# Performance work log

Measured on AMD Instinct MI355X. Metric: run time of the kernel, lower is better.

The kernel has to match this reference:

```python
import jax, jax.numpy as jnp
import numpy as np

# dims (match init_kwargs / input_specs)
D = 768      # embed_dim
H = 12       # num query heads
G = 4        # num kv groups
E = 8        # num experts
K = 2        # experts per token
F = 4 * D    # ffn hidden dim
B, S, T = 2, 1024, 1024
DH = D // H  # head dim = 64
EPS = 1e-6


def setup_inputs() -> dict:
    key = jax.random.key(0)
    ks = jax.random.split(key, 16)

    def p(k, shape, scale=0.02):
        return jax.random.normal(k, shape, jnp.float32) * scale

    inp = {}
    inp['x'] = jax.random.normal(ks[0], (B, S, D), jnp.float32)
    inp['encoder_context'] = jax.random.normal(ks[1], (B, T, D), jnp.float32)
    for n in ('ln1', 'ln2', 'ln3'):
        inp[n + '_scale'] = jnp.ones((D,), jnp.float32)
        inp[n + '_bias'] = jnp.zeros((D,), jnp.float32)
    i = 2
    for pre in ('sa', 'ca'):
        inp[pre + '_wq'] = p(ks[i], (D, H * DH)); i += 1
        inp[pre + '_bq'] = jnp.zeros((H * DH,), jnp.float32)
        inp[pre + '_wk'] = p(ks[i], (D, G * DH)); i += 1
        inp[pre + '_bk'] = jnp.zeros((G * DH,), jnp.float32)
        inp[pre + '_wv'] = p(ks[i], (D, G * DH)); i += 1
        inp[pre + '_bv'] = jnp.zeros((G * DH,), jnp.float32)
        inp[pre + '_wo'] = p(ks[i], (H * DH, D)); i += 1
        inp[pre + '_bo'] = jnp.zeros((D,), jnp.float32)
    inp['gate_w'] = p(ks[i], (D, E)); i += 1
    inp['gate_b'] = jnp.zeros((E,), jnp.float32)
    inp['w1'] = p(ks[i], (E, D, F)); i += 1
    inp['b1'] = jnp.zeros((E, F), jnp.float32)
    inp['w2'] = p(ks[i], (E, F, D)); i += 1
    inp['b2'] = jnp.zeros((E, D), jnp.float32)
    return inp


def _ln(x, scale, bias):
    mu = jnp.mean(x, axis=-1, keepdims=True)
    var = jnp.mean(jnp.square(x - mu), axis=-1, keepdims=True)
    return (x - mu) * jax.lax.rsqrt(var + EPS) * scale + bias


def _gqa(q_in, kv_in, wq, bq, wk, bk, wv, bv, wo, bo, causal):
    Bq, Sq, _ = q_in.shape
    Skv = kv_in.shape[1]
    q = (q_in @ wq + bq).reshape(Bq, Sq, H, DH)
    k = (kv_in @ wk + bk).reshape(Bq, Skv, G, DH)
    v = (kv_in @ wv + bv).reshape(Bq, Skv, G, DH)
    rep = H // G
    k = jnp.repeat(k, rep, axis=2)  # [B,Skv,H,DH]
    v = jnp.repeat(v, rep, axis=2)
    scores = jnp.einsum('bqhd,bkhd->bhqk', q, k) / jnp.sqrt(jnp.asarray(DH, q.dtype))
    if causal:
        cmask = jnp.tril(jnp.ones((Sq, Skv), bool))
        scores = jnp.where(cmask[None, None], scores, jnp.finfo(scores.dtype).min)
    attn = jax.nn.softmax(scores, axis=-1)
    out = jnp.einsum('bhqk,bkhd->bqhd', attn, v).reshape(Bq, Sq, H * DH)
    return out @ wo + bo


def _moe(x, gate_w, gate_b, w1, b1, w2, b2):
    logits = x @ gate_w + gate_b                      # [B,S,E]
    probs = jax.nn.softmax(logits, axis=-1)
    top_v, top_i = jax.lax.top_k(probs, K)            # [B,S,K]
    top_v = top_v / jnp.sum(top_v, axis=-1, keepdims=True)
    combine = jnp.sum(jax.nn.one_hot(top_i, E, dtype=x.dtype) * top_v[..., None], axis=-2)  # [B,S,E]
    h = jax.nn.gelu(jnp.einsum('bsd,edf->ebsf', x, w1) + b1[:, None, None, :])
    y = jnp.einsum('ebsf,efd->ebsd', h, w2) + b2[:, None, None, :]
    return jnp.einsum('ebsd,bse->bsd', y, combine)


def reference(x, encoder_context,
              ln1_scale, ln1_bias, ln2_scale, ln2_bias, ln3_scale, ln3_bias,
              sa_wq, sa_bq, sa_wk, sa_bk, sa_wv, sa_bv, sa_wo, sa_bo,
              ca_wq, ca_bq, ca_wk, ca_bk, ca_wv, ca_bv, ca_wo, ca_bo,
              gate_w, gate_b, w1, b1, w2, b2):
    xn = _ln(x, ln1_scale, ln1_bias)
    x = x + _gqa(xn, xn, sa_wq, sa_bq, sa_wk, sa_bk, sa_wv, sa_bv, sa_wo, sa_bo, causal=True)
    xn = _ln(x, ln2_scale, ln2_bias)
    x = x + _gqa(xn, encoder_context, ca_wq, ca_bq, ca_wk, ca_bk, ca_wv, ca_bv, ca_wo, ca_bo, causal=False)
    xn = _ln(x, ln3_scale, ln3_bias)
    x = x + _moe(xn, gate_w, gate_b, w1, b1, w2, b2)
    return x
```

## Files before the change

### kernel.cpp

```cpp
#include <hip/hip_runtime.h>

#define DEV __device__ __forceinline__

typedef __attribute__((ext_vector_type(4))) float f32x4;
typedef __attribute__((ext_vector_type(8))) short short8;
typedef __attribute__((ext_vector_type(4))) unsigned int u32x4;
typedef __attribute__((ext_vector_type(4))) unsigned short us16x4;

#define D_ 768
#define S_ 1024
#define B_ 2
#define H_ 12
#define G_ 4
#define DH_ 64
#define E_ 8
#define F_ 3072
#define NTOK (B_*S_)

#define GLDS16(g, l) __builtin_amdgcn_global_load_lds( \
    (const __attribute__((address_space(1))) void*)(g), \
    (__attribute__((address_space(3))) void*)(l), 16, 0, 0)

DEV unsigned short f2bf(float f){
  unsigned int b = __float_as_uint(f);
  b += 0x7FFFu + ((b >> 16) & 1u);
  return (unsigned short)(b >> 16);
}
DEV float bf2f(unsigned short h){ return __uint_as_float(((unsigned int)h) << 16); }
DEV unsigned int splitbf_pack(float v){
  unsigned short h = f2bf(v);
  unsigned short l = f2bf(v - bf2f(h));
  return (unsigned int)h | ((unsigned int)l << 16);
}

DEV short8 lds_swz(const unsigned short* base, int row, int chunk){
  return *(const short8*)((const char*)base + row*128 + (((chunk ^ (row & 7)) << 4)));
}
DEV short8 lds_swz32(const unsigned short* base, int row, int chunk){
  return *(const short8*)((const char*)base + row*64 + (((chunk ^ (row & 3)) << 4)));
}

DEV void swz_decode(int Fb, int nPanels, int& m, int& panel){
  int xcd = Fb & 7;
  int a = Fb >> 3;
  int mi = a & 3;
  int pid = (a >> 2)*8 + xcd;
  m = (pid / nPanels)*4 + mi;
  panel = pid % nPanels;
}

__global__ __launch_bounds__(256) void tcast_kernel(const float* __restrict__ W,
                                                    unsigned short* __restrict__ Wh,
                                                    unsigned short* __restrict__ Wl,
                                                    int K, int N){
  __shared__ float tile[32][33];
  long long zoff = (long long)blockIdx.z * K * N;
  const float* Wz = W + zoff;
  int n0 = blockIdx.x*32, k0 = blockIdx.y*32;
  int tx = threadIdx.x, ty = threadIdx.y;
  #pragma unroll
  for (int i=0;i<4;i++){
    int r = ty + i*8;
    tile[r][tx] = Wz[(long long)(k0+r)*N + n0 + tx];
  }
  __syncthreads();
  #pragma unroll
  for (int i=0;i<4;i++){
    int r = ty + i*8;
    float v = tile[tx][r];
    unsigned int hl = splitbf_pack(v);
    long long o = zoff + (long long)(n0+r)*K + k0 + tx;
    Wh[o] = (unsigned short)(hl & 0xFFFFu);
    if (Wl) Wl[o] = (unsigned short)(hl >> 16);
  }
}

struct TC4 {
  const float* s[4];
  unsigned short* h[4];
  unsigned short* l[4];
};
__global__ __launch_bounds__(256) void tcast4_kernel(TC4 tc, int K, int N){
  __shared__ float tile[32][33];
  int zi = blockIdx.z;
  const float* Wz = tc.s[zi];
  unsigned short* Wh = tc.h[zi];
  unsigned short* Wl = tc.l[zi];
  int n0 = blockIdx.x*32, k0 = blockIdx.y*32;
  int tx = threadIdx.x, ty = threadIdx.y;
  #pragma unroll
  for (int i=0;i<4;i++){
    int r = ty + i*8;
    tile[r][tx] = Wz[(long long)(k0+r)*N + n0 + tx];
  }
  __syncthreads();
  #pragma unroll
  for (int i=0;i<4;i++){
    int r = ty + i*8;
    float v = tile[tx][r];
    unsigned int hl = splitbf_pack(v);
    long long o = (long long)(n0+r)*K + k0 + tx;
    Wh[o] = (unsigned short)(hl & 0xFFFFu);
    Wl[o] = (unsigned short)(hl >> 16);
  }
}

__global__ void split_rows(const float* __restrict__ in, int ld, int width,
                           unsigned short* __restrict__ hi, unsigned short* __restrict__ lo){
  long long t = blockIdx.x;
  int c = threadIdx.x*4;
  f32x4 v = *(const f32x4*)(in + t*ld + c);
  unsigned int p0 = splitbf_pack(v.x), p1 = splitbf_pack(v.y);
  unsigned int p2 = splitbf_pack(v.z), p3 = splitbf_pack(v.w);
  us16x4 h, l;
  h.x=(unsigned short)p0; l.x=(unsigned short)(p0>>16);
  h.y=(unsigned short)p1; l.y=(unsigned short)(p1>>16);
  h.z=(unsigned short)p2; l.z=(unsigned short)(p2>>16);
  h.w=(unsigned short)p3; l.w=(unsigned short)(p3>>16);
  *(us16x4*)(hi + t*width + c) = h;
  *(us16x4*)(lo + t*width + c) = l;
}

__global__ void concat_bias(const float* __restrict__ b0, int n0,
                            const float* __restrict__ b1, int n1,
                            const float* __restrict__ b2, int n2,
                            float* __restrict__ out){
  int i = blockIdx.x*256 + threadIdx.x;
  if (i < n0) out[i] = b0[i];
  else if (i < n0+n1) out[i] = b1[i-n0];
  else if (i < n0+n1+n2) out[i] = b2[i-n0-n1];
}

__global__ __launch_bounds__(256) void ln_kernel(const float* __restrict__ x,
                                                 const float* __restrict__ sc,
                                                 const float* __restrict__ bi,
                                                 unsigned short* __restrict__ outh,
                                                 unsigned short* __restrict__ outl,
                                                 float* __restrict__ outf){
  __shared__ float red[8];
  long long row = blockIdx.x;
  const float* xr = x + row*D_;
  int tid = threadIdx.x;
  float v0 = xr[tid], v1 = xr[tid+256], v2 = xr[tid+512];
  float s = v0+v1+v2;
  float q = v0*v0 + v1*v1 + v2*v2;
  #pragma unroll
  for (int off=32; off; off>>=1){ s += __shfl_xor(s, off); q += __shfl_xor(q, off); }
  int lane = tid & 63, w = tid >> 6;
  if (lane == 0){ red[w] = s; red[4+w] = q; }
  __syncthreads();
  s = red[0]+red[1]+red[2]+red[3];
  q = red[4]+red[5]+red[6]+red[7];
  float mu  = s * (1.0f/D_);
  float var = q * (1.0f/D_) - mu*mu;
  float rstd = rsqrtf(var + 1e-6f);
  #pragma unroll
  for (int i=0;i<3;i++){
    int idx = tid + 256*i;
    float vv = (i==0) ? v0 : (i==1) ? v1 : v2;
    float o = (vv - mu)*rstd*sc[idx] + bi[idx];
    unsigned int pk = splitbf_pack(o);
    outh[row*D_ + idx] = (unsigned short)(pk & 0xFFFFu);
    if (outl) outl[row*D_ + idx] = (unsigned short)(pk >> 16);
    if (outf) outf[row*D_ + idx] = o;
  }
}

__global__ __launch_bounds__(256) void gemm3(
    int nX,
    const unsigned short* __restrict__ Ah, const unsigned short* __restrict__ Al, int lda,
    const unsigned short* __restrict__ Wh, const unsigned short* __restrict__ Wl, int K,
    const float* __restrict__ bias,
    const float* __restrict__ resid, int ldr,
    float* __restrict__ Cf, int ldc)
{
  __shared__ __align__(16) unsigned short AshH[128*64];
  __shared__ __align__(16) unsigned short AshL[128*64];
  __shared__ __align__(16) unsigned short BshH[64*64];
  __shared__ __align__(16) unsigned short BshL[64*64];
  int mB, panel;
  swz_decode(blockIdx.x, nX, mB, panel);
  const int r0 = mB*128;
  const int n0 = panel*64;
  const int tid = threadIdx.x;
  const int lane = tid & 63;
  const int wv = tid >> 6;
  const int wr = (wv>>1)*64, wc = (wv&1)*32;
  const int l15 = lane & 15, l4 = lane >> 4;
  const int sr = lane >> 3;
  const int sc = (lane & 7) ^ sr;

  f32x4 acc[4][2];
  #pragma unroll
  for (int i=0;i<4;i++)
    #pragma unroll
    for (int j=0;j<2;j++) acc[i][j] = (f32x4){0.f,0.f,0.f,0.f};

  for (int k0 = 0; k0 < K; k0 += 64){
    #pragma unroll
    for (int i=0;i<4;i++){
      int seg = wv*4 + i;
      long long src = (long long)(r0 + seg*8 + sr)*lda + k0 + sc*8;
      GLDS16(Ah + src, AshH + seg*8*64);
      GLDS16(Al + src, AshL + seg*8*64);
    }
    #pragma unroll
    for (int i=0;i<2;i++){
      int seg = wv*2 + i;
      long long src = (long long)(n0 + seg*8 + sr)*K + k0 + sc*8;
      GLDS16(Wh + src, BshH + seg*8*64);
      GLDS16(Wl + src, BshL + seg*8*64);
    }
    __syncthreads();
    #pragma unroll
    for (int ks=0; ks<2; ks++){
      int chunk = ks*4 + l4;
      short8 bh[2], bl[2];
      #pragma unroll
      for (int fj=0; fj<2; fj++){
        bh[fj] = lds_swz(BshH, wc + fj*16 + l15, chunk);
        bl[fj] = lds_swz(BshL, wc + fj*16 + l15, chunk);
      }
      #pragma unroll
      for (int fi=0; fi<4; fi++){
        short8 ah = lds_swz(AshH, wr + fi*16 + l15, chunk);
        short8 al = lds_swz(AshL, wr + fi*16 + l15, chunk);
        #pragma unroll
        for (int fj=0; fj<2; fj++){
          acc[fi][fj] = __builtin_amdgcn_mfma_f32_16x16x32_bf16(ah, bh[fj], acc[fi][fj], 0,0,0);
          acc[fi][fj] = __builtin_amdgcn_mfma_f32_16x16x32_bf16(al, bh[fj], acc[fi][fj], 0,0,0);
          acc[fi][fj] = __builtin_amdgcn_mfma_f32_16x16x32_bf16(ah, bl[fj], acc[fi][fj], 0,0,0);
        }
      }
    }
    __syncthreads();
  }

  #pragma unroll
  for (int fi=0; fi<4; fi++)
  #pragma unroll
  for (int fj=0; fj<2; fj++)
  #pragma unroll
  for (int reg=0; reg<4; reg++){
    int r = r0 + wr + fi*16 + l4*4 + reg;
    int col = n0 + wc + fj*16 + l15;
    float val = acc[fi][fj][reg] + bias[col];
    if (resid) val += resid[(long long)r*ldr + col];
    Cf[(long long)r*ldc + col] = val;
  }
}

__global__ __launch_bounds__(256) void gemm_nt128(
    int nX, int nzPerE,
    const unsigned short* __restrict__ A, int lda,
    const unsigned short* __restrict__ Wt, long long wstride,
    const float* __restrict__ bias, int bias_stride,
    const int* __restrict__ counts,
    const int* __restrict__ a_idx, int a_idx_stride,
    const int* __restrict__ row_base,
    float* __restrict__ Cf, long long partStride,
    unsigned short* __restrict__ Cb, int ldc,
    int K, int do_gelu)
{
  __shared__ __align__(16) unsigned short As[2][128*32];
  __shared__ __align__(16) unsigned short Bs[2][128*32];
  int mB, panel;
  swz_decode(blockIdx.x, nX*E_*nzPerE, mB, panel);
  const int n0 = (panel % nX)*128;
  const int zI = panel / nX;
  const int z = zI / nzPerE;
  const int kp = zI % nzPerE;
  const int Mz = counts[z];
  const int r0 = mB*128;
  if (r0 >= Mz) return;
  const int obase = row_base[z];
  const unsigned short* Wz = Wt + (long long)z*wstride;
  const float* bz = bias + (long long)z*bias_stride;
  const int kLen = K / nzPerE;
  const int kBeg = kp * kLen;
  const int tid = threadIdx.x;
  const int lane = tid & 63;
  const int wv = tid >> 6;
  const int wr = (wv>>1)*64, wc = (wv&1)*64;
  const int l15 = lane & 15, l4 = lane >> 4;
  const int r16 = lane >> 2;
  const int sc4 = (lane & 3) ^ (r16 & 3);

  long long arow[2];
  #pragma unroll
  for (int i=0;i<2;i++){
    int seg = wv*2 + i;
    int r = r0 + seg*16 + r16;
    int rcl = (r < Mz) ? r : (Mz-1);
    arow[i] = a_idx ? (long long)a_idx[(long long)z*a_idx_stride + rcl]
                    : (long long)(obase + rcl);
  }

  f32x4 acc[4][4];
  #pragma unroll
  for (int i=0;i<4;i++)
    #pragma unroll
    for (int j=0;j<4;j++) acc[i][j] = (f32x4){0.f,0.f,0.f,0.f};

  auto stage = [&](int buf, int k0){
    #pragma unroll
    for (int i=0;i<2;i++){
      int seg = wv*2 + i;
      GLDS16(A + arow[i]*lda + k0 + sc4*8, &As[buf][seg*512]);
      GLDS16(Wz + (long long)(n0 + seg*16 + r16)*K + k0 + sc4*8, &Bs[buf][seg*512]);
    }
  };

  const int nsteps = kLen >> 5;
  stage(0, kBeg);
  int cur = 0;
  for (int t=0; t<nsteps; t++){
    if (t+1 < nsteps){
      stage(cur^1, kBeg + (t+1)*32);
      asm volatile("s_waitcnt vmcnt(4)" ::: "memory");
    } else {
      asm volatile("s_waitcnt vmcnt(0)" ::: "memory");
    }
    __builtin_amdgcn_s_barrier();
    __builtin_amdgcn_sched_barrier(0);
    {
      short8 a[4], b[4];
      #pragma unroll
      for (int f=0; f<4; f++){
        a[f] = lds_swz32(&As[cur][0], wr + f*16 + l15, l4);
        b[f] = lds_swz32(&Bs[cur][0], wc + f*16 + l15, l4);
      }
      #pragma unroll
      for (int fi=0; fi<4; fi++)
        #pragma unroll
        for (int fj=0; fj<4; fj++)
          acc[fi][fj] = __builtin_amdgcn_mfma_f32_16x16x32_bf16(a[fi], b[fj], acc[fi][fj], 0,0,0);
    }
    __builtin_amdgcn_s_barrier();
    cur ^= 1;
  }

  #pragma unroll
  for (int fi=0; fi<4; fi++)
  #pragma unroll
  for (int fj=0; fj<4; fj++)
  #pragma unroll
  for (int reg=0; reg<4; reg++){
    int r = r0 + wr + fi*16 + l4*4 + reg;
    if (r >= Mz) continue;
    int col = n0 + wc + fj*16 + l15;
    float val = acc[fi][fj][reg] + (kp == 0 ? bz[col] : 0.0f);
    if (do_gelu){
      float xx = val;
      float u = 0.7978845608028654f*(xx + 0.044715f*xx*xx*xx);
      float t = 1.0f - 2.0f/(__expf(2.0f*u) + 1.0f);
      val = 0.5f*xx*(1.0f + t);
    }
    long long orow = (long long)obase + r;
    if (Cf) Cf[kp*partStride + orow*ldc + col] = val;
    if (Cb) Cb[orow*ldc + col] = f2bf(val);
  }
}

__global__ __launch_bounds__(256) void vt_split_kernel(const float* __restrict__ vin,
                                                       int ld, int cofs,
                                                       unsigned short* __restrict__ vth,
                                                       unsigned short* __restrict__ vtl){
  __shared__ float tile[32][33];
  int s0 = blockIdx.x*32, d0 = blockIdx.y*32;
  int bg = blockIdx.z; int b = bg >> 2, g = bg & 3;
  int tx = threadIdx.x, ty = threadIdx.y;
  #pragma unroll
  for (int i=0;i<4;i++){
    int r = ty + i*8;
    tile[r][tx] = vin[(long long)(b*1024 + s0 + r)*ld + cofs + g*64 + d0 + tx];
  }
  __syncthreads();
  #pragma unroll
  for (int i=0;i<4;i++){
    int d = d0 + ty + i*8;
    unsigned int pk = splitbf_pack(tile[tx][ty + i*8]);
    long long o = (long long)(bg*64 + d)*1024 + s0 + tx;
    vth[o] = (unsigned short)(pk & 0xFFFFu);
    vtl[o] = (unsigned short)(pk >> 16);
  }
}

#define AT_LDP 76
__global__ __launch_bounds__(256, 2) void attn_mfma(
    const float* __restrict__ q, int qld,
    const unsigned short* __restrict__ kh, const unsigned short* __restrict__ kl,
    const unsigned short* __restrict__ vth, const unsigned short* __restrict__ vtl,
    unsigned short* __restrict__ ctxh, unsigned short* __restrict__ ctxl, int causal)
{
  __shared__ __align__(16) unsigned short KhS[64*64];
  __shared__ __align__(16) unsigned short KlS[64*64];
  __shared__ __align__(16) unsigned short VhS[64*64];
  __shared__ __align__(16) unsigned short VlS[64*64];
  __shared__ __align__(16) unsigned int   Pp[4][16*AT_LDP];

  const int qblk = blockIdx.x;
  const int h = blockIdx.y;
  const int b = blockIdx.z;
  const int g = h / (H_/G_);
  const int tid = threadIdx.x;
  const int lane = tid & 63;
  const int w = tid >> 6;
  const int l15 = lane & 15;
  const int l4 = lane >> 4;
  const int sr = lane >> 3;
  const int sc = (lane & 7) ^ sr;
  const int qb0 = qblk*64;

  short8 qh[2], ql[2];
  #pragma unroll
  for (int ks=0; ks<2; ks++){
    const float* qp = q + ((long long)(b*S_ + qb0 + w*16 + l15))*qld + h*DH_ + ks*32 + l4*8;
    f32x4 q0 = *(const f32x4*)qp;
    f32x4 q1 = *(const f32x4*)(qp + 4);
    float qq[8] = {q0.x,q0.y,q0.z,q0.w,q1.x,q1.y,q1.z,q1.w};
    #pragma unroll
    for (int j=0;j<8;j++){
      unsigned int pk = splitbf_pack(qq[j]*0.125f);
      qh[ks][j] = (short)(pk & 0xFFFFu);
      ql[ks][j] = (short)(pk >> 16);
    }
  }

  f32x4 o[4];
  #pragma unroll
  for (int fd=0; fd<4; fd++) o[fd] = (f32x4){0.f,0.f,0.f,0.f};
  float m[4]    = {-3.0e38f,-3.0e38f,-3.0e38f,-3.0e38f};
  float lsum[4] = {0.f,0.f,0.f,0.f};

  const int ntiles = causal ? (qblk + 1) : (S_/64);
  for (int kt=0; kt<ntiles; kt++){
    __syncthreads();
    #pragma unroll
    for (int i=0;i<2;i++){
      int seg = w*2 + i;
      int row = seg*8 + sr;
      long long ksrc = (long long)(b*S_ + kt*64 + row)*(G_*DH_) + g*DH_ + sc*8;
      long long vsrc = (long long)((b*G_ + g)*64 + row)*S_ + kt*64 + sc*8;
      GLDS16(kh  + ksrc, KhS + seg*8*64);
      GLDS16(kl  + ksrc, KlS + seg*8*64);
      GLDS16(vth + vsrc, VhS + seg*8*64);
      GLDS16(vtl + vsrc, VlS + seg*8*64);
    }
    __syncthreads();

    f32x4 s[4];
    #pragma unroll
    for (int fj=0; fj<4; fj++) s[fj] = (f32x4){0.f,0.f,0.f,0.f};
    #pragma unroll
    for (int ks=0; ks<2; ks++){
      int chunk = ks*4 + l4;
      #pragma unroll
      for (int fj=0; fj<4; fj++){
        short8 bh = lds_swz(KhS, fj*16 + l15, chunk);
        short8 bl = lds_swz(KlS, fj*16 + l15, chunk);
        s[fj] = __builtin_amdgcn_mfma_f32_16x16x32_bf16(qh[ks], bh, s[fj], 0,0,0);
        s[fj] = __builtin_amdgcn_mfma_f32_16x16x32_bf16(ql[ks], bh, s[fj], 0,0,0);
        s[fj] = __builtin_amdgcn_mfma_f32_16x16x32_bf16(qh[ks], bl, s[fj], 0,0,0);
      }
    }

    if (causal && kt == qblk){
      #pragma unroll
      for (int fj=0; fj<4; fj++){
        int key = kt*64 + fj*16 + l15;
        #pragma unroll
        for (int reg=0; reg<4; reg++){
          int qr = qb0 + w*16 + l4*4 + reg;
          if (key > qr) s[fj][reg] = -3.0e38f;
        }
      }
    }

    float c[4], pmax[4];
    #pragma unroll
    for (int reg=0; reg<4; reg++){
      float mx = fmaxf(fmaxf(s[0][reg], s[1][reg]), fmaxf(s[2][reg], s[3][reg]));
      mx = fmaxf(mx, __shfl_xor(mx, 1));
      mx = fmaxf(mx, __shfl_xor(mx, 2));
      mx = fmaxf(mx, __shfl_xor(mx, 4));
      mx = fmaxf(mx, __shfl_xor(mx, 8));
      float mn = fmaxf(m[reg], mx);
      c[reg] = __expf(m[reg] - mn);
      m[reg] = mn;
      pmax[reg] = mn;
    }
    float psum[4] = {0.f,0.f,0.f,0.f};
    #pragma unroll
    for (int fj=0; fj<4; fj++){
      #pragma unroll
      for (int reg=0; reg<4; reg++){
        float pv = __expf(s[fj][reg] - pmax[reg]);
        psum[reg] += pv;
        Pp[w][(l4*4 + reg)*AT_LDP + fj*16 + l15] = splitbf_pack(pv);
      }
    }
    #pragma unroll
    for (int reg=0; reg<4; reg++){
      float ps = psum[reg];
      ps += __shfl_xor(ps, 1); ps += __shfl_xor(ps, 2);
      ps += __shfl_xor(ps, 4); ps += __shfl_xor(ps, 8);
      lsum[reg] = lsum[reg]*c[reg] + ps;
      o[0][reg] *= c[reg]; o[1][reg] *= c[reg];
      o[2][reg] *= c[reg]; o[3][reg] *= c[reg];
    }

    #pragma unroll
    for (int ks=0; ks<2; ks++){
      int chunk = ks*4 + l4;
      u32x4 pa = *(const u32x4*)&Pp[w][l15*AT_LDP + ks*32 + l4*8];
      u32x4 pb = *(const u32x4*)&Pp[w][l15*AT_LDP + ks*32 + l4*8 + 4];
      short8 ph, pl;
      #pragma unroll
      for (int j=0;j<4;j++){
        ph[j]   = (short)(pa[j] & 0xFFFFu); pl[j]   = (short)(pa[j] >> 16);
        ph[4+j] = (short)(pb[j] & 0xFFFFu); pl[4+j] = (short)(pb[j] >> 16);
      }
      #pragma unroll
      for (int fd=0; fd<4; fd++){
        short8 vh = lds_swz(VhS, fd*16 + l15, chunk);
        short8 vl = lds_swz(VlS, fd*16 + l15, chunk);
        o[fd] = __builtin_amdgcn_mfma_f32_16x16x32_bf16(ph, vh, o[fd], 0,0,0);
        o[fd] = __builtin_amdgcn_mfma_f32_16x16x32_bf16(pl, vh, o[fd], 0,0,0);
        o[fd] = __builtin_amdgcn_mfma_f32_16x16x32_bf16(ph, vl, o[fd], 0,0,0);
      }
    }
  }

  #pragma unroll
  for (int reg=0; reg<4; reg++){
    float inv = 1.0f / lsum[reg];
    long long tok = b*S_ + qb0 + w*16 + l4*4 + reg;
    #pragma unroll
    for (int fd=0; fd<4; fd++){
      unsigned int pk = splitbf_pack(o[fd][reg]*inv);
      long long oidx = tok*D_ + h*DH_ + fd*16 + l15;
      ctxh[oidx] = (unsigned short)(pk & 0xFFFFu);
      ctxl[oidx] = (unsigned short)(pk >> 16);
    }
  }
}

__global__ __launch_bounds__(256) void gate_kernel(const float* __restrict__ xnf,
                                                   const float* __restrict__ gw,
                                                   const float* __restrict__ gb,
                                                   int* __restrict__ counts,
                                                   int* __restrict__ toklist,
                                                   int* __restrict__ route_e,
                                                   int* __restrict__ route_pos,
                                                   float* __restrict__ route_w){
  int t = blockIdx.x*4 + (threadIdx.x >> 6);
  int lane = threadIdx.x & 63;
  float acc[E_];
  #pragma unroll
  for (int e=0;e<E_;e++) acc[e] = 0.f;
  #pragma unroll
  for (int i=0;i<12;i++){
    int d = lane + 64*i;
    float xv = xnf[(long long)t*D_ + d];
    const float* w = gw + (long long)d*E_;
    #pragma unroll
    for (int e=0;e<E_;e++) acc[e] += xv*w[e];
  }
  #pragma unroll
  for (int off=32; off; off>>=1)
    #pragma unroll
    for (int e=0;e<E_;e++) acc[e] += __shfl_xor(acc[e], off);
  if (lane == 0){
    #pragma unroll
    for (int e=0;e<E_;e++) acc[e] += gb[e];
    int e0 = 0;
    #pragma unroll
    for (int e=1;e<E_;e++) if (acc[e] > acc[e0]) e0 = e;
    int e1 = -1;
    #pragma unroll
    for (int e=0;e<E_;e++) if (e != e0 && (e1 < 0 || acc[e] > acc[e1])) e1 = e;
    float w0 = 1.0f/(1.0f + __expf(acc[e1] - acc[e0]));
    float w1 = 1.0f - w0;
    int p0 = atomicAdd(&counts[e0], 1);
    int p1 = atomicAdd(&counts[e1], 1);
    toklist[e0*NTOK + p0] = t;
    toklist[e1*NTOK + p1] = t;
    route_e[2*t]   = e0; route_e[2*t+1]   = e1;
    route_pos[2*t] = p0; route_pos[2*t+1] = p1;
    route_w[2*t]   = w0; route_w[2*t+1]   = w1;
  }
}

__global__ void offsets_kernel(const int* __restrict__ counts, int* __restrict__ offs){
  if (threadIdx.x == 0){
    int s = 0;
    for (int e=0;e<E_;e++){ offs[e] = s; s += counts[e]; }
  }
}

__global__ __launch_bounds__(192) void combine_kernel(const float* __restrict__ xb,
                                                      const float* __restrict__ y,
                                                      long long partStride,
                                                      const int* __restrict__ route_e,
                                                      const int* __restrict__ route_pos,
                                                      const float* __restrict__ route_w,
                                                      const int* __restrict__ offs,
                                                      float* __restrict__ out){
  int t = blockIdx.x;
  int i = threadIdx.x;
  int e0 = route_e[2*t], e1 = route_e[2*t+1];
  long long s0 = offs[e0] + route_pos[2*t];
  long long s1 = offs[e1] + route_pos[2*t+1];
  float w0 = route_w[2*t], w1 = route_w[2*t+1];
  f32x4 xv = *(const f32x4*)(xb + (long long)t*D_ + i*4);
  f32x4 y0 = (f32x4){0.f,0.f,0.f,0.f};
  f32x4 y1 = (f32x4){0.f,0.f,0.f,0.f};
  #pragma unroll
  for (int kp=0; kp<2; kp++){
    y0 += *(const f32x4*)(y + kp*partStride + s0*D_ + i*4);
    y1 += *(const f32x4*)(y + kp*partStride + s1*D_ + i*4);
  }
  f32x4 o = xv + w0*y0 + w1*y1;
  *(f32x4*)(out + (long long)t*D_ + i*4) = o;
}

extern "C" void kernel_launch(void* const* d_in, const int* in_sizes, int n_in,
                              void* d_out, int out_size, void* d_ws, size_t ws_size,
                              hipStream_t stream) {
  (void)in_sizes; (void)n_in; (void)out_size; (void)ws_size;
  const float* x     = (const float*)d_in[0];
  const float* enc   = (const float*)d_in[1];
  const float* ln1s  = (const float*)d_in[2];
  const float* ln1b  = (const float*)d_in[3];
  const float* ln2s  = (const float*)d_in[4];
  const float* ln2b  = (const float*)d_in[5];
  const float* ln3s  = (const float*)d_in[6];
  const float* ln3b  = (const float*)d_in[7];
  const float* sa_wq = (const float*)d_in[8];
  const float* sa_bq = (const float*)d_in[9];
  const float* sa_wk = (const float*)d_in[10];
  const float* sa_bk = (const float*)d_in[11];
  const float* sa_wv = (const float*)d_in[12];
  const float* sa_bv = (const float*)d_in[13];
  const float* sa_wo = (const float*)d_in[14];
  const float* sa_bo = (const float*)d_in[15];
  const float* ca_wq = (const float*)d_in[16];
  const float* ca_bq = (const float*)d_in[17];
  const float* ca_wk = (const float*)d_in[18];
  const float* ca_bk = (const float*)d_in[19];
  const float* ca_wv = (const float*)d_in[20];
  const float* ca_bv = (const float*)d_in[21];
  const float* ca_wo = (const float*)d_in[22];
  const float* ca_bo = (const float*)d_in[23];
  const float* gate_w= (const float*)d_in[24];
  const float* gate_b= (const float*)d_in[25];
  const float* w1    = (const float*)d_in[26];
  const float* b1    = (const float*)d_in[27];
  const float* w2    = (const float*)d_in[28];
  const float* b2    = (const float*)d_in[29];
  float* out = (float*)d_out;

  char* p = (char*)d_ws;
  auto alloc = [&](size_t bytes)->void*{
    void* r = (void*)p;
    p += (bytes + 255) & ~(size_t)255;
    return r;
  };
  unsigned short* wqkvh_sa = (unsigned short*)alloc((size_t)1280*768*2);
  unsigned short* wqkvl_sa = (unsigned short*)alloc((size_t)1280*768*2);
  unsigned short* woh_sa   = (unsigned short*)alloc((size_t)768*768*2);
  unsigned short* wol_sa   = (unsigned short*)alloc((size_t)768*768*2);
  unsigned short* wqh_ca   = (unsigned short*)alloc((size_t)768*768*2);
  unsigned short* wql_ca   = (unsigned short*)alloc((size_t)768*768*2);
  unsigned short* wkvh_ca  = (unsigned short*)alloc((size_t)512*768*2);
  unsigned short* wkvl_ca  = (unsigned short*)alloc((size_t)512*768*2);
  unsigned short* woh_ca   = (unsigned short*)alloc((size_t)768*768*2);
  unsigned short* wol_ca   = (unsigned short*)alloc((size_t)768*768*2);
  unsigned short* w1T = (unsigned short*)alloc((size_t)E_*D_*F_*2);
  unsigned short* w2T = (unsigned short*)alloc((size_t)E_*D_*F_*2);
  float* bqkv_sa = (float*)alloc(1280*4);
  float* bkv_ca  = (float*)alloc(512*4);
  unsigned short* ench = (unsigned short*)alloc((size_t)NTOK*D_*2);
  unsigned short* encl = (unsigned short*)alloc((size_t)NTOK*D_*2);
  unsigned short* xh   = (unsigned short*)alloc((size_t)NTOK*D_*2);
  unsigned short* xl   = (unsigned short*)alloc((size_t)NTOK*D_*2);
  unsigned short* ctxh = (unsigned short*)alloc((size_t)NTOK*D_*2);
  unsigned short* ctxl = (unsigned short*)alloc((size_t)NTOK*D_*2);
  unsigned short* xn_b = (unsigned short*)alloc((size_t)NTOK*D_*2);
  unsigned short* hbuf = (unsigned short*)alloc((size_t)2*NTOK*F_*2);
  unsigned short* khp   = (unsigned short*)alloc((size_t)NTOK*G_*DH_*2);
  unsigned short* klp   = (unsigned short*)alloc((size_t)NTOK*G_*DH_*2);
  unsigned short* vtp_h = (unsigned short*)alloc((size_t)NTOK*G_*DH_*2);
  unsigned short* vtp_l = (unsigned short*)alloc((size_t)NTOK*G_*DH_*2);
  float* qkvbuf = (float*)alloc((size_t)NTOK*1280*4);
  float* xnf  = (float*)alloc((size_t)NTOK*D_*4);
  float* xbuf = (float*)alloc((size_t)NTOK*D_*4);
  float* ybuf = (float*)alloc((size_t)4*NTOK*D_*4);
  int* counts    = (int*)alloc(E_*4);
  int* offs      = (int*)alloc(E_*4);
  int* toklist   = (int*)alloc((size_t)E_*NTOK*4);
  int* route_e   = (int*)alloc((size_t)2*NTOK*4);
  int* route_pos = (int*)alloc((size_t)2*NTOK*4);
  float* route_w = (float*)alloc((size_t)2*NTOK*4);

  (void)hipMemsetAsync(counts, 0, E_*sizeof(int), stream);

  dim3 tb(32,8);
  {
    TC4 a;
    a.s[0]=sa_wq; a.h[0]=wqkvh_sa;           a.l[0]=wqkvl_sa;
    a.s[1]=sa_wo; a.h[1]=woh_sa;             a.l[1]=wol_sa;
    a.s[2]=ca_wq; a.h[2]=wqh_ca;             a.l[2]=wql_ca;
    a.s[3]=ca_wo; a.h[3]=woh_ca;             a.l[3]=wol_ca;
    tcast4_kernel<<<dim3(24,24,4), tb, 0, stream>>>(a, 768, 768);
    TC4 b;
    b.s[0]=sa_wk; b.h[0]=wqkvh_sa + 768*768;  b.l[0]=wqkvl_sa + 768*768;
    b.s[1]=sa_wv; b.h[1]=wqkvh_sa + 1024*768; b.l[1]=wqkvl_sa + 1024*768;
    b.s[2]=ca_wk; b.h[2]=wkvh_ca;             b.l[2]=wkvl_ca;
    b.s[3]=ca_wv; b.h[3]=wkvh_ca + 256*768;   b.l[3]=wkvl_ca + 256*768;
    tcast4_kernel<<<dim3(8,24,4), tb, 0, stream>>>(b, 768, 256);
  }
  tcast_kernel<<<dim3(96,24,E_), tb, 0, stream>>>(w1, w1T, nullptr, 768, 3072);
  tcast_kernel<<<dim3(24,96,E_), tb, 0, stream>>>(w2, w2T, nullptr, 3072, 768);
  concat_bias<<<5, 256, 0, stream>>>(sa_bq, 768, sa_bk, 256, sa_bv, 256, bqkv_sa);
  concat_bias<<<2, 256, 0, stream>>>(ca_bk, 256, ca_bv, 256, nullptr, 0, bkv_ca);
  split_rows<<<NTOK, 192, 0, stream>>>(enc, 768, 768, ench, encl);

  ln_kernel<<<NTOK, 256, 0, stream>>>(x, ln1s, ln1b, xh, xl, nullptr);
  gemm3<<<20*16, 256, 0, stream>>>(20, xh, xl, 768, wqkvh_sa, wqkvl_sa, 768,
      bqkv_sa, nullptr, 0, qkvbuf, 1280);
  split_rows<<<NTOK, 64, 0, stream>>>(qkvbuf + 768, 1280, 256, khp, klp);
  vt_split_kernel<<<dim3(32,2,8), tb, 0, stream>>>(qkvbuf, 1280, 1024, vtp_h, vtp_l);
  attn_mfma<<<dim3(16,12,2), 256, 0, stream>>>(qkvbuf, 1280, khp, klp, vtp_h, vtp_l, ctxh, ctxl, 1);
  gemm3<<<12*16, 256, 0, stream>>>(12, ctxh, ctxl, 768, woh_sa, wol_sa, 768,
      sa_bo, x, 768, xbuf, 768);

  ln_kernel<<<NTOK, 256, 0, stream>>>(xbuf, ln2s, ln2b, xh, xl, nullptr);
  gemm3<<<12*16, 256, 0, stream>>>(12, xh, xl, 768, wqh_ca, wql_ca, 768,
      ca_bq, nullptr, 0, qkvbuf, 1280);
  gemm3<<<8*16, 256, 0, stream>>>(8, ench, encl, 768, wkvh_ca, wkvl_ca, 768,
      bkv_ca, nullptr, 0, qkvbuf + 768, 1280);
  split_rows<<<NTOK, 64, 0, stream>>>(qkvbuf + 768, 1280, 256, khp, klp);
  vt_split_kernel<<<dim3(32,2,8), tb, 0, stream>>>(qkvbuf, 1280, 1024, vtp_h, vtp_l);
  attn_mfma<<<dim3(16,12,2), 256, 0, stream>>>(qkvbuf, 1280, khp, klp, vtp_h, vtp_l, ctxh, ctxl, 0);
  gemm3<<<12*16, 256, 0, stream>>>(12, ctxh, ctxl, 768, woh_ca, wol_ca, 768,
      ca_bo, xbuf, 768, xbuf, 768);

  ln_kernel<<<NTOK, 256, 0, stream>>>(xbuf, ln3s, ln3b, xn_b, nullptr, xnf);
  gate_kernel<<<NTOK/4, 256, 0, stream>>>(xnf, gate_w, gate_b,
      counts, toklist, route_e, route_pos, route_w);
  offsets_kernel<<<1, 64, 0, stream>>>(counts, offs);
  gemm_nt128<<<24*16*E_, 256, 0, stream>>>(24, 1, xn_b, 768, w1T, (long long)F_*D_, b1, F_,
      counts, toklist, NTOK, offs, nullptr, 0, hbuf, F_, 768, 1);
  long long partStride = (long long)2*NTOK*D_;
  gemm_nt128<<<6*16*E_*2, 256, 0, stream>>>(6, 2, hbuf, F_, w2T, (long long)F_*D_, b2, D_,
      counts, nullptr, 0, offs, ybuf, partStride, nullptr, 768, F_, 0);
  combine_kernel<<<NTOK, 192, 0, stream>>>(xbuf, ybuf, partStride,
      route_e, route_pos, route_w, offs, out);
}
```

Baseline: 493.9 us.

## Fuse K/V split and V transpose into QKV GEMM epilogue, merge cross-attn projections

The QKV GEMM epilogue now writes Q as fp32 and K/V directly as split bf16 hi/lo, with V stored transposed. This removes the separate split_rows and vt_split kernels and the fp32 qkv staging buffer. The cross-attention Q and encoder-KV GEMMs are merged into one launch that picks operands per panel. The offsets kernel is dropped and each block recomputes prefix sums from counts instead. The V-transposed stores in the epilogue are scattered and uncoalesced, and there is a dead bias expression left in the code.

```diff
diff --git a/kernel.cpp b/kernel.cpp
--- a/kernel.cpp
+++ b/kernel.cpp
@@ -167,12 +167,19 @@
 }
 
 __global__ __launch_bounds__(256) void gemm3(
-    int nX,
-    const unsigned short* __restrict__ Ah, const unsigned short* __restrict__ Al, int lda,
-    const unsigned short* __restrict__ Wh, const unsigned short* __restrict__ Wl, int K,
-    const float* __restrict__ bias,
+    int nX, int nQ,
+    const unsigned short* __restrict__ A0h, const unsigned short* __restrict__ A0l, int lda0,
+    const unsigned short* __restrict__ W0h, const unsigned short* __restrict__ W0l,
+    const float* __restrict__ bias0,
+    const unsigned short* __restrict__ A1h, const unsigned short* __restrict__ A1l, int lda1,
+    const unsigned short* __restrict__ W1h, const unsigned short* __restrict__ W1l,
+    const float* __restrict__ bias1,
+    int K, int mode,
     const float* __restrict__ resid, int ldr,
-    float* __restrict__ Cf, int ldc)
+    float* __restrict__ Cf, int ldc,
+    float* __restrict__ qout,
+    unsigned short* __restrict__ kh, unsigned short* __restrict__ kl,
+    unsigned short* __restrict__ vth, unsigned short* __restrict__ vtl)
 {
   __shared__ __align__(16) unsigned short AshH[128*64];
   __shared__ __align__(16) unsigned short AshL[128*64];
@@ -181,7 +188,6 @@
   int mB, panel;
   swz_decode(blockIdx.x, nX, mB, panel);
   const int r0 = mB*128;
-  const int n0 = panel*64;
   const int tid = threadIdx.x;
   const int lane = tid & 63;
   const int wv = tid >> 6;
@@ -190,6 +196,17 @@
   const int sr = lane >> 3;
   const int sc = (lane & 7) ^ sr;
 
+  const unsigned short *Ah, *Al, *Wh, *Wl;
+  const float* bias;
+  int lda, wn0, colbase;
+  if (panel < nQ){
+    Ah = A0h; Al = A0l; lda = lda0; Wh = W0h; Wl = W0l; bias = bias0;
+    wn0 = panel*64; colbase = panel*64;
+  } else {
+    Ah = A1h; Al = A1l; lda = lda1; Wh = W1h; Wl = W1l; bias = bias1;
+    wn0 = (panel - nQ)*64; colbase = 768 + (panel - nQ)*64;
+  }
+
   f32x4 acc[4][2];
   #pragma unroll
   for (int i=0;i<4;i++)
@@ -207,7 +224,7 @@
     #pragma unroll
     for (int i=0;i<2;i++){
       int seg = wv*2 + i;
-      long long src = (long long)(n0 + seg*8 + sr)*K + k0 + sc*8;
+      long long src = (long long)(wn0 + seg*8 + sr)*K + k0 + sc*8;
       GLDS16(Wh + src, BshH + seg*8*64);
       GLDS16(Wl + src, BshL + seg*8*64);
     }
@@ -243,10 +260,36 @@
   #pragma unroll
   for (int reg=0; reg<4; reg++){
     int r = r0 + wr + fi*16 + l4*4 + reg;
-    int col = n0 + wc + fj*16 + l15;
-    float val = acc[fi][fj][reg] + bias[col];
-    if (resid) val += resid[(long long)r*ldr + col];
-    Cf[(long long)r*ldc + col] = val;
+    int lcol = colbase + wc + fj*16 + l15;
+    float bval = (lcol < 768) ? bias0[ (panel<nQ && mode==1) ? lcol : (wn0 + wc + fj*16 + l15) ]
+                              : bias1 ? bias1[lcol-768] : bias0[lcol];
+    float val;
+    if (mode == 0){
+      val = acc[fi][fj][reg] + bias0[wn0 + wc + fj*16 + l15];
+      if (resid) val += resid[(long long)r*ldr + (wn0 + wc + fj*16 + l15)];
+      Cf[(long long)r*ldc + (wn0 + wc + fj*16 + l15)] = val;
+    } else {
+      if (lcol < 768){
+        val = acc[fi][fj][reg] + bias0[lcol];
+        qout[(long long)r*768 + lcol] = val;
+      } else {
+        val = acc[fi][fj][reg] + ((panel < nQ) ? bias0[lcol] : bias1[lcol-768]);
+        unsigned int pk = splitbf_pack(val);
+        int c2 = lcol - 768;
+        if (c2 < 256){
+          kh[(long long)r*256 + c2] = (unsigned short)(pk & 0xFFFFu);
+          kl[(long long)r*256 + c2] = (unsigned short)(pk >> 16);
+        } else {
+          int d = c2 - 256;
+          int g = d >> 6, dd = d & 63;
+          int b = r >> 10, ss = r & 1023;
+          long long o = ((long long)((b*G_ + g)*64 + dd))*1024 + ss;
+          vth[o] = (unsigned short)(pk & 0xFFFFu);
+          vtl[o] = (unsigned short)(pk >> 16);
+        }
+      }
+    }
+    (void)bval;
   }
 }
 
@@ -257,7 +300,6 @@
     const float* __restrict__ bias, int bias_stride,
     const int* __restrict__ counts,
     const int* __restrict__ a_idx, int a_idx_stride,
-    const int* __restrict__ row_base,
     float* __restrict__ Cf, long long partStride,
     unsigned short* __restrict__ Cb, int ldc,
     int K, int do_gelu)
@@ -273,7 +315,8 @@
   const int Mz = counts[z];
   const int r0 = mB*128;
   if (r0 >= Mz) return;
-  const int obase = row_base[z];
+  int obase = 0;
+  for (int e=0;e<z;e++) obase += counts[e];
   const unsigned short* Wz = Wt + (long long)z*wstride;
   const float* bz = bias + (long long)z*bias_stride;
   const int kLen = K / nzPerE;
@@ -359,30 +402,6 @@
     long long orow = (long long)obase + r;
     if (Cf) Cf[kp*partStride + orow*ldc + col] = val;
     if (Cb) Cb[orow*ldc + col] = f2bf(val);
-  }
-}
-
-__global__ __launch_bounds__(256) void vt_split_kernel(const float* __restrict__ vin,
-                                                       int ld, int cofs,
-                                                       unsigned short* __restrict__ vth,
-                                                       unsigned short* __restrict__ vtl){
-  __shared__ float tile[32][33];
-  int s0 = blockIdx.x*32, d0 = blockIdx.y*32;
-  int bg = blockIdx.z; int b = bg >> 2, g = bg & 3;
-  int tx = threadIdx.x, ty = threadIdx.y;
-  #pragma unroll
-  for (int i=0;i<4;i++){
-    int r = ty + i*8;
-    tile[r][tx] = vin[(long long)(b*1024 + s0 + r)*ld + cofs + g*64 + d0 + tx];
-  }
-  __syncthreads();
-  #pragma unroll
-  for (int i=0;i<4;i++){
-    int d = d0 + ty + i*8;
-    unsigned int pk = splitbf_pack(tile[tx][ty + i*8]);
-    long long o = (long long)(bg*64 + d)*1024 + s0 + tx;
-    vth[o] = (unsigned short)(pk & 0xFFFFu);
-    vtl[o] = (unsigned short)(pk >> 16);
   }
 }
 
@@ -592,26 +611,24 @@
   }
 }
 
-__global__ void offsets_kernel(const int* __restrict__ counts, int* __restrict__ offs){
-  if (threadIdx.x == 0){
-    int s = 0;
-    for (int e=0;e<E_;e++){ offs[e] = s; s += counts[e]; }
-  }
-}
-
 __global__ __launch_bounds__(192) void combine_kernel(const float* __restrict__ xb,
                                                       const float* __restrict__ y,
                                                       long long partStride,
+                                                      const int* __restrict__ counts,
                                                       const int* __restrict__ route_e,
                                                       const int* __restrict__ route_pos,
                                                       const float* __restrict__ route_w,
-                                                      const int* __restrict__ offs,
                                                       float* __restrict__ out){
   int t = blockIdx.x;
   int i = threadIdx.x;
   int e0 = route_e[2*t], e1 = route_e[2*t+1];
-  long long s0 = offs[e0] + route_pos[2*t];
-  long long s1 = offs[e1] + route_pos[2*t+1];
+  int off0 = 0, off1 = 0;
+  for (int e=0;e<E_;e++){
+    if (e < e0) off0 += counts[e];
+    if (e < e1) off1 += counts[e];
+  }
+  long long s0 = off0 + route_pos[2*t];
+  long long s1 = off1 + route_pos[2*t+1];
   float w0 = route_w[2*t], w1 = route_w[2*t+1];
   f32x4 xv = *(const f32x4*)(xb + (long long)t*D_ + i*4);
   f32x4 y0 = (f32x4){0.f,0.f,0.f,0.f};
@@ -693,12 +710,11 @@
   unsigned short* klp   = (unsigned short*)alloc((size_t)NTOK*G_*DH_*2);
   unsigned short* vtp_h = (unsigned short*)alloc((size_t)NTOK*G_*DH_*2);
   unsigned short* vtp_l = (unsigned short*)alloc((size_t)NTOK*G_*DH_*2);
-  float* qkvbuf = (float*)alloc((size_t)NTOK*1280*4);
+  float* qbuf = (float*)alloc((size_t)NTOK*D_*4);
   float* xnf  = (float*)alloc((size_t)NTOK*D_*4);
   float* xbuf = (float*)alloc((size_t)NTOK*D_*4);
   float* ybuf = (float*)alloc((size_t)4*NTOK*D_*4);
   int* counts    = (int*)alloc(E_*4);
-  int* offs      = (int*)alloc(E_*4);
   int* toklist   = (int*)alloc((size_t)E_*NTOK*4);
   int* route_e   = (int*)alloc((size_t)2*NTOK*4);
   int* route_pos = (int*)alloc((size_t)2*NTOK*4);
@@ -728,34 +744,39 @@
   split_rows<<<NTOK, 192, 0, stream>>>(enc, 768, 768, ench, encl);
 
   ln_kernel<<<NTOK, 256, 0, stream>>>(x, ln1s, ln1b, xh, xl, nullptr);
-  gemm3<<<20*16, 256, 0, stream>>>(20, xh, xl, 768, wqkvh_sa, wqkvl_sa, 768,
-      bqkv_sa, nullptr, 0, qkvbuf, 1280);
-  split_rows<<<NTOK, 64, 0, stream>>>(qkvbuf + 768, 1280, 256, khp, klp);
-  vt_split_kernel<<<dim3(32,2,8), tb, 0, stream>>>(qkvbuf, 1280, 1024, vtp_h, vtp_l);
-  attn_mfma<<<dim3(16,12,2), 256, 0, stream>>>(qkvbuf, 1280, khp, klp, vtp_h, vtp_l, ctxh, ctxl, 1);
-  gemm3<<<12*16, 256, 0, stream>>>(12, ctxh, ctxl, 768, woh_sa, wol_sa, 768,
-      sa_bo, x, 768, xbuf, 768);
+  gemm3<<<20*16, 256, 0, stream>>>(20, 20,
+      xh, xl, 768, wqkvh_sa, wqkvl_sa, bqkv_sa,
+      nullptr, nullptr, 0, nullptr, nullptr, nullptr,
+      768, 1, nullptr, 0, nullptr, 0,
+      qbuf, khp, klp, vtp_h, vtp_l);
+  attn_mfma<<<dim3(16,12,2), 256, 0, stream>>>(qbuf, 768, khp, klp, vtp_h, vtp_l, ctxh, ctxl, 1);
+  gemm3<<<12*16, 256, 0, stream>>>(12, 12,
+      ctxh, ctxl, 768, woh_sa, wol_sa, sa_bo,
+      nullptr, nullptr, 0, nullptr, nullptr, nullptr,
+      768, 0, x, 768, xbuf, 768,
+      nullptr, nullptr, nullptr, nullptr, nullptr);
 
   ln_kernel<<<NTOK, 256, 0, stream>>>(xbuf, ln2s, ln2b, xh, xl, nullptr);
-  gemm3<<<12*16, 256, 0, stream>>>(12, xh, xl, 768, wqh_ca, wql_ca, 768,
-      ca_bq, nullptr, 0, qkvbuf, 1280);
-  gemm3<<<8*16, 256, 0, stream>>>(8, ench, encl, 768, wkvh_ca, wkvl_ca, 768,
-      bkv_ca, nullptr, 0, qkvbuf + 768, 1280);
-  split_rows<<<NTOK, 64, 0, stream>>>(qkvbuf + 768, 1280, 256, khp, klp);
-  vt_split_kernel<<<dim3(32,2,8), tb, 0, stream>>>(qkvbuf, 1280, 1024, vtp_h, vtp_l);
-  attn_mfma<<<dim3(16,12,2), 256, 0, stream>>>(qkvbuf, 1280, khp, klp, vtp_h, vtp_l, ctxh, ctxl, 0);
-  gemm3<<<12*16, 256, 0, stream>>>(12, ctxh, ctxl, 768, woh_ca, wol_ca, 768,
-      ca_bo, xbuf, 768, xbuf, 768);
+  gemm3<<<20*16, 256, 0, stream>>>(20, 12,
+      xh, xl, 768, wqh_ca, wql_ca, ca_bq,
+      ench, encl, 768, wkvh_ca, wkvl_ca, bkv_ca,
+      768, 1, nullptr, 0, nullptr, 0,
+      qbuf, khp, klp, vtp_h, vtp_l);
+  attn_mfma<<<dim3(16,12,2), 256, 0, stream>>>(qbuf, 768, khp, klp, vtp_h, vtp_l, ctxh, ctxl, 0);
+  gemm3<<<12*16, 256, 0, stream>>>(12, 12,
+      ctxh, ctxl, 768, woh_ca, wol_ca, ca_bo,
+      nullptr, nullptr, 0, nullptr, nullptr, nullptr,
+      768, 0, xbuf, 768, xbuf, 768,
+      nullptr, nullptr, nullptr, nullptr, nullptr);
 
   ln_kernel<<<NTOK, 256, 0, stream>>>(xbuf, ln3s, ln3b, xn_b, nullptr, xnf);
   gate_kernel<<<NTOK/4, 256, 0, stream>>>(xnf, gate_w, gate_b,
       counts, toklist, route_e, route_pos, route_w);
-  offsets_kernel<<<1, 64, 0, stream>>>(counts, offs);
   gemm_nt128<<<24*16*E_, 256, 0, stream>>>(24, 1, xn_b, 768, w1T, (long long)F_*D_, b1, F_,
-      counts, toklist, NTOK, offs, nullptr, 0, hbuf, F_, 768, 1);
+      counts, toklist, NTOK, nullptr, 0, hbuf, F_, 768, 1);
   long long partStride = (long long)2*NTOK*D_;
   gemm_nt128<<<6*16*E_*2, 256, 0, stream>>>(6, 2, hbuf, F_, w2T, (long long)F_*D_, b2, D_,
-      counts, nullptr, 0, offs, ybuf, partStride, nullptr, 768, F_, 0);
+      counts, nullptr, 0, ybuf, partStride, nullptr, 768, F_, 0);
   combine_kernel<<<NTOK, 192, 0, stream>>>(xbuf, ybuf, partStride,
-      route_e, route_pos, route_w, offs, out);
-}
+      counts, route_e, route_pos, route_w, out);
+}
```

Measured after the change: 505.1 us. 2.3% more time.
